# Kernel tuning notes

Hardware: AMD Instinct MI355X
Metric: run time of the kernel (lower is better)

Reference implementation:

```python
import jax, jax.numpy as jnp
import numpy as np

TEMPERATURE = 0.07


def _l2_normalize(x, axis=-1, eps=1e-12):
    # matches torch F.normalize: x / max(||x||, eps)
    n = jnp.sqrt(jnp.sum(x * x, axis=axis, keepdims=True))
    return x / jnp.maximum(n, eps)


def setup_inputs() -> dict:
    key = jax.random.key(0)
    k1, k2, k3 = jax.random.split(key, 3)
    B, C, H, W = 1024, 256, 24, 24
    img_features = jax.random.normal(k1, (B, C, H, W), dtype=jnp.float32)
    text_embeds = jax.random.normal(k2, (B, C), dtype=jnp.float32)
    labels = jax.random.randint(k3, (B,), 0, 16, dtype=jnp.int64)
    return {"img_features": img_features, "text_embeds": text_embeds, "labels": labels}


def reference(img_features, text_embeds, labels):
    # adaptive_avg_pool2d to 1x1 == global mean over H,W -> [B, C]
    img_pooled = img_features.mean(axis=(2, 3))
    img_pooled = _l2_normalize(img_pooled, axis=1)
    text_n = _l2_normalize(text_embeds, axis=1)
    logits = (img_pooled @ text_n.T) / TEMPERATURE  # [B, B]
    # vectorized label equality replaces the O(N^2) python loop
    targets = (labels[:, None] == labels[None, :]).astype(logits.dtype)
    # BCE with logits, mean reduction: logaddexp(0, x) - x*z
    loss = jnp.mean(jnp.logaddexp(0.0, logits) - logits * targets)
    return loss
```

## Files before the change

### kernel.cpp

```cpp
#include <hip/hip_runtime.h>
#include <math.h>

static constexpr int B_N  = 1024;
static constexpr int C_N  = 256;
static constexpr int HW_N = 576;
static constexpr float TEMP_INV = 1.0f / 0.07f;

__global__ __launch_bounds__(256) void pool_kernel(const float* __restrict__ img,
                                                   float* __restrict__ pooled) {
    const int wave = threadIdx.x >> 6;
    const int lane = threadIdx.x & 63;
    const size_t row = (size_t)blockIdx.x * 4 + wave;
    const float4* src = (const float4*)(img + row * HW_N);

    float s = 0.0f;
    #pragma unroll
    for (int it = 0; it < 3; ++it) {
        int idx = lane + it * 64;
        if (idx < 144) {
            float4 v = src[idx];
            s += (v.x + v.y) + (v.z + v.w);
        }
    }
    #pragma unroll
    for (int off = 32; off > 0; off >>= 1) s += __shfl_xor(s, off, 64);
    if (lane == 0) pooled[row] = s * (1.0f / (float)HW_N);
}

__global__ __launch_bounds__(256) void norm_kernel(const float* __restrict__ pooled,
                                                   const float* __restrict__ text,
                                                   float* __restrict__ inv_img,
                                                   float* __restrict__ inv_text,
                                                   float* __restrict__ loss_acc) {
    if (blockIdx.x == 0 && threadIdx.x == 0) *loss_acc = 0.0f;

    const int wave = threadIdx.x >> 6;
    const int lane = threadIdx.x & 63;
    const int r = blockIdx.x * 4 + wave;
    const float* srcbase = (r < B_N) ? (pooled + (size_t)r * C_N)
                                     : (text   + (size_t)(r - B_N) * C_N);
    const float4 v = ((const float4*)srcbase)[lane];
    float ss = v.x * v.x + v.y * v.y + v.z * v.z + v.w * v.w;
    #pragma unroll
    for (int off = 32; off > 0; off >>= 1) ss += __shfl_xor(ss, off, 64);
    if (lane == 0) {
        float inv = 1.0f / fmaxf(sqrtf(ss), 1e-12f);
        if (r < B_N) inv_img[r] = inv;
        else         inv_text[r - B_N] = inv;
    }
}

__global__ __launch_bounds__(256) void gemm_loss_kernel(const float* __restrict__ pooled,
                                                        const float* __restrict__ text,
                                                        const float* __restrict__ inv_img,
                                                        const float* __restrict__ inv_text,
                                                        const int* __restrict__ labels,
                                                        float* __restrict__ loss_acc) {
    __shared__ float As[64][36];
    __shared__ float Bs[32][68];

    const int t  = threadIdx.x;
    const int tx = t & 15;
    const int ty = t >> 4;
    const int rowBase = (blockIdx.x & 15) * 64;
    const int colBase = (blockIdx.x >> 4) * 64;

    float c[4][4] = {{0.f}};

    for (int kb = 0; kb < C_N; kb += 32) {
        #pragma unroll
        for (int s = 0; s < 2; ++s) {
            const int f4  = t + s * 256;
            const int row = f4 >> 3;
            const int kq  = f4 & 7;
            float4 va = *(const float4*)(pooled + (size_t)(rowBase + row) * C_N + kb + kq * 4);
            *(float4*)&As[row][kq * 4] = va;
            float4 vb = *(const float4*)(text + (size_t)(colBase + row) * C_N + kb + kq * 4);
            Bs[kq * 4 + 0][row] = vb.x;
            Bs[kq * 4 + 1][row] = vb.y;
            Bs[kq * 4 + 2][row] = vb.z;
            Bs[kq * 4 + 3][row] = vb.w;
        }
        __syncthreads();

        #pragma unroll
        for (int k4 = 0; k4 < 8; ++k4) {
            float4 a[4], b[4];
            #pragma unroll
            for (int i = 0; i < 4; ++i) a[i] = *(const float4*)&As[ty * 4 + i][k4 * 4];
            #pragma unroll
            for (int kk = 0; kk < 4; ++kk) b[kk] = *(const float4*)&Bs[k4 * 4 + kk][tx * 4];
            #pragma unroll
            for (int i = 0; i < 4; ++i) {
                const float* ap = (const float*)&a[i];
                #pragma unroll
                for (int kk = 0; kk < 4; ++kk) {
                    const float* bp = (const float*)&b[kk];
                    c[i][0] += ap[kk] * bp[0];
                    c[i][1] += ap[kk] * bp[1];
                    c[i][2] += ap[kk] * bp[2];
                    c[i][3] += ap[kk] * bp[3];
                }
            }
        }
        __syncthreads();
    }

    float lsum = 0.0f;
    #pragma unroll
    for (int i = 0; i < 4; ++i) {
        const int gi = rowBase + ty * 4 + i;
        const float si = inv_img[gi] * TEMP_INV;
        const int li = labels[gi];
        #pragma unroll
        for (int j = 0; j < 4; ++j) {
            const int gj = colBase + tx * 4 + j;
            const float x = c[i][j] * si * inv_text[gj];
            const float z = (li == labels[gj]) ? 1.0f : 0.0f;
            const float sp = fmaxf(x, 0.0f) + log1pf(expf(-fabsf(x)));
            lsum += sp - x * z;
        }
    }

    #pragma unroll
    for (int off = 32; off > 0; off >>= 1) lsum += __shfl_xor(lsum, off, 64);
    __syncthreads();
    float* red = &As[0][0];
    if ((t & 63) == 0) red[t >> 6] = lsum;
    __syncthreads();
    if (t == 0) {
        float bsum = red[0] + red[1] + red[2] + red[3];
        atomicAdd(loss_acc, bsum);
    }
}

__global__ void finalize_kernel(const float* __restrict__ loss_acc,
                                float* __restrict__ out) {
    out[0] = loss_acc[0] * (1.0f / ((float)B_N * (float)B_N));
}

extern "C" void kernel_launch(void* const* d_in, const int* in_sizes, int n_in,
                              void* d_out, int out_size, void* d_ws, size_t ws_size,
                              hipStream_t stream) {
    const float* img    = (const float*)d_in[0];
    const float* text   = (const float*)d_in[1];
    const int*   labels = (const int*)d_in[2];
    float* out = (float*)d_out;

    char* ws = (char*)d_ws;
    float* pooled   = (float*)ws;
    float* inv_img  = (float*)(ws + (1 << 20));
    float* inv_text = (float*)(ws + (1 << 20) + 4096);
    float* loss_acc = (float*)(ws + (1 << 20) + 8192);

    pool_kernel<<<(B_N * C_N) / 4, 256, 0, stream>>>(img, pooled);
    norm_kernel<<<(2 * B_N) / 4, 256, 0, stream>>>(pooled, text, inv_img, inv_text, loss_acc);
    gemm_loss_kernel<<<256, 256, 0, stream>>>(pooled, text, inv_img, inv_text, labels, loss_acc);
    finalize_kernel<<<1, 1, 0, stream>>>(loss_acc, out);
}
```

Before: 126.9 us.

## Use bf16 MFMA for similarity GEMM with pre-normalized operands and fused finalize

The normalize kernel now writes L2-normalized rows converted to bf16, and the GEMM loads whole 64x256 bf16 tiles into swizzled shared memory and computes them with 16x16x32 bf16 MFMA instructions instead of scalar fp32 FMAs. The separate finalize kernel is removed: the last GEMM block, found through an atomic ticket counter, writes the mean. The pool kernel takes over zeroing the accumulator and ticket. The main cost is still the 600MB pooling read, so the GEMM and launch savings are small, and bf16 rounding adds some error to the logits.

Result: faster. 118.9 us (-6.3%).

```diff
diff --git a/kernel.cpp b/kernel.cpp
--- a/kernel.cpp
+++ b/kernel.cpp
@@ -6,8 +6,20 @@
 static constexpr int HW_N = 576;
 static constexpr float TEMP_INV = 1.0f / 0.07f;
 
+typedef __attribute__((ext_vector_type(8))) short bf16x8;
+typedef __attribute__((ext_vector_type(4))) float f32x4;
+
+static __device__ __forceinline__ unsigned short f2bf(float f) {
+    unsigned u = __float_as_uint(f);
+    return (unsigned short)((u + 0x7FFFu + ((u >> 16) & 1u)) >> 16);
+}
+
 __global__ __launch_bounds__(256) void pool_kernel(const float* __restrict__ img,
-                                                   float* __restrict__ pooled) {
+                                                   float* __restrict__ pooled,
+                                                   float* __restrict__ loss_acc,
+                                                   unsigned int* __restrict__ ticket) {
+    if (blockIdx.x == 0 && threadIdx.x == 0) { *loss_acc = 0.0f; *ticket = 0u; }
+
     const int wave = threadIdx.x >> 6;
     const int lane = threadIdx.x & 63;
     const size_t row = (size_t)blockIdx.x * 4 + wave;
@@ -27,96 +39,91 @@
     if (lane == 0) pooled[row] = s * (1.0f / (float)HW_N);
 }
 
-__global__ __launch_bounds__(256) void norm_kernel(const float* __restrict__ pooled,
+__global__ __launch_bounds__(256) void prep_kernel(const float* __restrict__ pooled,
                                                    const float* __restrict__ text,
-                                                   float* __restrict__ inv_img,
-                                                   float* __restrict__ inv_text,
-                                                   float* __restrict__ loss_acc) {
-    if (blockIdx.x == 0 && threadIdx.x == 0) *loss_acc = 0.0f;
-
+                                                   unsigned short* __restrict__ Ab,
+                                                   unsigned short* __restrict__ Bb) {
     const int wave = threadIdx.x >> 6;
     const int lane = threadIdx.x & 63;
     const int r = blockIdx.x * 4 + wave;
-    const float* srcbase = (r < B_N) ? (pooled + (size_t)r * C_N)
-                                     : (text   + (size_t)(r - B_N) * C_N);
-    const float4 v = ((const float4*)srcbase)[lane];
+    const float* src = (r < B_N) ? (pooled + (size_t)r * C_N)
+                                 : (text   + (size_t)(r - B_N) * C_N);
+    const float4 v = ((const float4*)src)[lane];
     float ss = v.x * v.x + v.y * v.y + v.z * v.z + v.w * v.w;
     #pragma unroll
     for (int off = 32; off > 0; off >>= 1) ss += __shfl_xor(ss, off, 64);
-    if (lane == 0) {
-        float inv = 1.0f / fmaxf(sqrtf(ss), 1e-12f);
-        if (r < B_N) inv_img[r] = inv;
-        else         inv_text[r - B_N] = inv;
-    }
+    const float inv = 1.0f / fmaxf(sqrtf(ss), 1e-12f);
+
+    ushort4 o;
+    o.x = f2bf(v.x * inv); o.y = f2bf(v.y * inv);
+    o.z = f2bf(v.z * inv); o.w = f2bf(v.w * inv);
+    unsigned short* dst = (r < B_N) ? (Ab + (size_t)r * C_N)
+                                    : (Bb + (size_t)(r - B_N) * C_N);
+    ((ushort4*)dst)[lane] = o;
 }
 
-__global__ __launch_bounds__(256) void gemm_loss_kernel(const float* __restrict__ pooled,
-                                                        const float* __restrict__ text,
-                                                        const float* __restrict__ inv_img,
-                                                        const float* __restrict__ inv_text,
+__global__ __launch_bounds__(256) void gemm_loss_kernel(const unsigned short* __restrict__ Ab,
+                                                        const unsigned short* __restrict__ Bb,
                                                         const int* __restrict__ labels,
-                                                        float* __restrict__ loss_acc) {
-    __shared__ float As[64][36];
-    __shared__ float Bs[32][68];
+                                                        float* __restrict__ loss_acc,
+                                                        unsigned int* __restrict__ ticket,
+                                                        float* __restrict__ out) {
+    __shared__ unsigned short Abuf[64 * 256];
+    __shared__ unsigned short Bbuf[64 * 256];
 
-    const int t  = threadIdx.x;
-    const int tx = t & 15;
-    const int ty = t >> 4;
-    const int rowBase = (blockIdx.x & 15) * 64;
-    const int colBase = (blockIdx.x >> 4) * 64;
+    const int t = threadIdx.x;
+    const int rowBase = (blockIdx.x & 15) << 6;
+    const int colBase = (blockIdx.x >> 4) << 6;
 
-    float c[4][4] = {{0.f}};
+    #pragma unroll
+    for (int i = 0; i < 8; ++i) {
+        const int c   = t + (i << 8);
+        const int row = c >> 5;
+        const int kc  = c & 31;
+        const unsigned off = (unsigned)((row << 9) + (kc << 4)) ^ (unsigned)((row & 7) << 4);
+        uint4 va = ((const uint4*)(Ab + (size_t)(rowBase + row) * C_N))[kc];
+        *(uint4*)((char*)Abuf + off) = va;
+        uint4 vb = ((const uint4*)(Bb + (size_t)(colBase + row) * C_N))[kc];
+        *(uint4*)((char*)Bbuf + off) = vb;
+    }
+    __syncthreads();
 
-    for (int kb = 0; kb < C_N; kb += 32) {
+    const int w    = t >> 6;
+    const int lane = t & 63;
+    const int m16  = lane & 15;
+    const int kg   = lane >> 4;
+
+    f32x4 acc[4] = {{0.f, 0.f, 0.f, 0.f}, {0.f, 0.f, 0.f, 0.f},
+                    {0.f, 0.f, 0.f, 0.f}, {0.f, 0.f, 0.f, 0.f}};
+
+    #pragma unroll
+    for (int s = 0; s < 8; ++s) {
+        const int kc   = (s << 2) + kg;
+        const int arow = (w << 4) + m16;
+        const bf16x8 a = *(const bf16x8*)((char*)Abuf +
+                            (((unsigned)((arow << 9) + (kc << 4))) ^ (unsigned)((arow & 7) << 4)));
         #pragma unroll
-        for (int s = 0; s < 2; ++s) {
-            const int f4  = t + s * 256;
-            const int row = f4 >> 3;
-            const int kq  = f4 & 7;
-            float4 va = *(const float4*)(pooled + (size_t)(rowBase + row) * C_N + kb + kq * 4);
-            *(float4*)&As[row][kq * 4] = va;
-            float4 vb = *(const float4*)(text + (size_t)(colBase + row) * C_N + kb + kq * 4);
-            Bs[kq * 4 + 0][row] = vb.x;
-            Bs[kq * 4 + 1][row] = vb.y;
-            Bs[kq * 4 + 2][row] = vb.z;
-            Bs[kq * 4 + 3][row] = vb.w;
+        for (int ct = 0; ct < 4; ++ct) {
+            const int brow = (ct << 4) + m16;
+            const bf16x8 b = *(const bf16x8*)((char*)Bbuf +
+                                (((unsigned)((brow << 9) + (kc << 4))) ^ (unsigned)((brow & 7) << 4)));
+            acc[ct] = __builtin_amdgcn_mfma_f32_16x16x32_bf16(a, b, acc[ct], 0, 0, 0);
         }
-        __syncthreads();
-
-        #pragma unroll
-        for (int k4 = 0; k4 < 8; ++k4) {
-            float4 a[4], b[4];
-            #pragma unroll
-            for (int i = 0; i < 4; ++i) a[i] = *(const float4*)&As[ty * 4 + i][k4 * 4];
-            #pragma unroll
-            for (int kk = 0; kk < 4; ++kk) b[kk] = *(const float4*)&Bs[k4 * 4 + kk][tx * 4];
-            #pragma unroll
-            for (int i = 0; i < 4; ++i) {
-                const float* ap = (const float*)&a[i];
-                #pragma unroll
-                for (int kk = 0; kk < 4; ++kk) {
-                    const float* bp = (const float*)&b[kk];
-                    c[i][0] += ap[kk] * bp[0];
-                    c[i][1] += ap[kk] * bp[1];
-                    c[i][2] += ap[kk] * bp[2];
-                    c[i][3] += ap[kk] * bp[3];
-                }
-            }
-        }
-        __syncthreads();
     }
 
     float lsum = 0.0f;
+    const int gi0 = rowBase + (w << 4) + (kg << 2);
+    int labi[4];
     #pragma unroll
-    for (int i = 0; i < 4; ++i) {
-        const int gi = rowBase + ty * 4 + i;
-        const float si = inv_img[gi] * TEMP_INV;
-        const int li = labels[gi];
+    for (int r = 0; r < 4; ++r) labi[r] = labels[gi0 + r];
+    #pragma unroll
+    for (int ct = 0; ct < 4; ++ct) {
+        const int gj = colBase + (ct << 4) + m16;
+        const int labj = labels[gj];
         #pragma unroll
-        for (int j = 0; j < 4; ++j) {
-            const int gj = colBase + tx * 4 + j;
-            const float x = c[i][j] * si * inv_text[gj];
-            const float z = (li == labels[gj]) ? 1.0f : 0.0f;
+        for (int r = 0; r < 4; ++r) {
+            const float x = acc[ct][r] * TEMP_INV;
+            const float z = (labi[r] == labj) ? 1.0f : 0.0f;
             const float sp = fmaxf(x, 0.0f) + log1pf(expf(-fabsf(x)));
             lsum += sp - x * z;
         }
@@ -125,18 +132,19 @@
     #pragma unroll
     for (int off = 32; off > 0; off >>= 1) lsum += __shfl_xor(lsum, off, 64);
     __syncthreads();
-    float* red = &As[0][0];
-    if ((t & 63) == 0) red[t >> 6] = lsum;
+    float* red = (float*)Abuf;
+    if ((t & 63) == 0) red[w] = lsum;
     __syncthreads();
     if (t == 0) {
-        float bsum = red[0] + red[1] + red[2] + red[3];
+        const float bsum = red[0] + red[1] + red[2] + red[3];
         atomicAdd(loss_acc, bsum);
+        __threadfence();
+        const unsigned old = atomicAdd(ticket, 1u);
+        if (old == 255u) {
+            const float total = atomicAdd(loss_acc, 0.0f);
+            out[0] = total * (1.0f / ((float)B_N * (float)B_N));
+        }
     }
-}
-
-__global__ void finalize_kernel(const float* __restrict__ loss_acc,
-                                float* __restrict__ out) {
-    out[0] = loss_acc[0] * (1.0f / ((float)B_N * (float)B_N));
 }
 
 extern "C" void kernel_launch(void* const* d_in, const int* in_sizes, int n_in,
@@ -148,13 +156,13 @@
     float* out = (float*)d_out;
 
     char* ws = (char*)d_ws;
-    float* pooled   = (float*)ws;
-    float* inv_img  = (float*)(ws + (1 << 20));
-    float* inv_text = (float*)(ws + (1 << 20) + 4096);
-    float* loss_acc = (float*)(ws + (1 << 20) + 8192);
+    float*          pooled   = (float*)ws;
+    unsigned short* Ab       = (unsigned short*)(ws + (1 << 20));
+    unsigned short* Bb       = (unsigned short*)(ws + (1 << 20) + (512 << 10));
+    float*          loss_acc = (float*)(ws + (2 << 20));
+    unsigned int*   ticket   = (unsigned int*)(ws + (2 << 20) + 4);
 
-    pool_kernel<<<(B_N * C_N) / 4, 256, 0, stream>>>(img, pooled);
-    norm_kernel<<<(2 * B_N) / 4, 256, 0, stream>>>(pooled, text, inv_img, inv_text, loss_acc);
-    gemm_loss_kernel<<<256, 256, 0, stream>>>(pooled, text, inv_img, inv_text, labels, loss_acc);
-    finalize_kernel<<<1, 1, 0, stream>>>(loss_acc, out);
+    pool_kernel<<<(B_N * C_N) / 4, 256, 0, stream>>>(img, pooled, loss_acc, ticket);
+    prep_kernel<<<(2 * B_N) / 4, 256, 0, stream>>>(pooled, text, Ab, Bb);
+    gemm_loss_kernel<<<256, 256, 0, stream>>>(Ab, Bb, labels, loss_acc, ticket, out);
 }
```
